# Optimization experiments

Hardware: AMD Instinct MI355X
Metric: run time of the kernel (lower is better)

The kernel has to match this reference:

```python
import jax, jax.numpy as jnp
import numpy as np

T, B, F = 160, 640, 40
HID, PROJ, LAYERS = 768, 256, 3


def lstm_proj_layer(x, Wk, b, Wp, reverse=False):
    # x: [T, B, in]; Wk: [in+PROJ, 4*HID]; b: [4*HID]; Wp: [HID, PROJ]
    nb = x.shape[1]
    c0 = jnp.zeros((nb, HID), x.dtype)
    h0 = jnp.zeros((nb, PROJ), x.dtype)

    def step(carry, xt):
        c, h = carry
        z = jnp.concatenate([xt, h], axis=-1) @ Wk + b
        i, j, f, o = jnp.split(z, 4, axis=-1)  # TF LSTMCell gate order i,j,f,o
        c = jax.nn.sigmoid(f + 1.0) * c + jax.nn.sigmoid(i) * jnp.tanh(j)  # forget_bias=1.0
        h = (jax.nn.sigmoid(o) * jnp.tanh(c)) @ Wp  # projection
        return (c, h), h

    _, ys = jax.lax.scan(step, (c0, h0), x, reverse=reverse)
    return ys  # [T, B, PROJ], time-aligned with input even when reverse=True


def _run_stack(x, params, reverse):
    for (Wk, b, Wp) in params:
        x = lstm_proj_layer(x, Wk, b, Wp, reverse=reverse)
    return x


def setup_inputs() -> dict:
    key = jax.random.key(0)
    keys = jax.random.split(key, 1 + 6 * LAYERS)
    inp = {"batch": jax.random.normal(keys[0], (T, B, F), dtype=jnp.float32)}
    ki = 1
    for d in ("fw", "bw"):
        for l in range(LAYERS):
            in_dim = F if l == 0 else PROJ
            inp[f"Wk_{d}{l}"] = jax.random.normal(keys[ki], (in_dim + PROJ, 4 * HID), dtype=jnp.float32) * 0.05
            inp[f"b_{d}{l}"] = jnp.zeros((4 * HID,), dtype=jnp.float32)
            inp[f"Wp_{d}{l}"] = jax.random.normal(keys[ki + 1], (HID, PROJ), dtype=jnp.float32) * 0.05
            ki += 2
    return inp


def reference(batch,
              Wk_fw0, b_fw0, Wp_fw0, Wk_fw1, b_fw1, Wp_fw1, Wk_fw2, b_fw2, Wp_fw2,
              Wk_bw0, b_bw0, Wp_bw0, Wk_bw1, b_bw1, Wp_bw1, Wk_bw2, b_bw2, Wp_bw2):
    fw_params = [(Wk_fw0, b_fw0, Wp_fw0), (Wk_fw1, b_fw1, Wp_fw1), (Wk_fw2, b_fw2, Wp_fw2)]
    bw_params = [(Wk_bw0, b_bw0, Wp_bw0), (Wk_bw1, b_bw1, Wp_bw1), (Wk_bw2, b_bw2, Wp_bw2)]
    out_fw = _run_stack(batch, fw_params, reverse=False)
    out_bw = _run_stack(batch, bw_params, reverse=True)
    outputs = jnp.concatenate([out_fw, out_bw], axis=2)  # [T, B, 2*PROJ]
    embedded = (outputs[0] + outputs[-1]) / 2.0
    # tf.nn.l2_normalize semantics
    embedded = embedded * jax.lax.rsqrt(jnp.maximum(jnp.sum(embedded * embedded, axis=-1, keepdims=True), 1e-12))
    return embedded
```

## Files before the change

### kernel.cpp

```cpp
#include <hip/hip_runtime.h>


typedef _Float16 h8 __attribute__((ext_vector_type(8)));
typedef float f4 __attribute__((ext_vector_type(4)));

#define T_STEPS 160
#define NB 640
#define HID 768
#define PROJ 256
#define NGATE 3072

__device__ __forceinline__ float sigm(float x) { return 1.0f / (1.0f + __expf(-x)); }
__device__ __forceinline__ float tanh_fast(float x) { return 2.0f / (1.0f + __expf(-2.0f * x)) - 1.0f; }

struct GateArgs {
  const _Float16* A0[6];
  const _Float16* A1[6];
  const _Float16* Bw[6];
  const float*    bias[6];
  float*          cst[6];
  _Float16*       g[6];
  int w0[6];
  int lda0[6];
  int K[6];
  int act[6];
};

struct ProjArgs {
  const _Float16* G[6];
  const _Float16* Wp[6];
  _Float16* out[6];
  _Float16* out2[6];
  int act[6];
};

__global__ __launch_bounds__(256, 3) void gate_step(GateArgs args) {
  const int z = blockIdx.z;
  if (!args.act[z]) return;

  __shared__ __align__(16) char sm[36864];
  _Float16 (*As)[72] = (_Float16(*)[72])sm;
  _Float16 (*Bs)[72] = (_Float16(*)[72])(sm + 18432);
  float (*zs)[65] = (float(*)[65])sm;

  const _Float16* A0 = args.A0[z];
  const _Float16* A1 = args.A1[z];
  const _Float16* Bw = args.Bw[z];
  const int w0 = args.w0[z], lda0 = args.lda0[z], K = args.K[z];
  const int n0 = blockIdx.x * 128;
  const int m0 = blockIdx.y * 128;
  const int tid = threadIdx.x;
  const int lane = tid & 63;
  const int wv = tid >> 6;
  const int wm = (wv & 1) * 64;
  const int wn = (wv >> 1) * 64;

  const float* bias = args.bias[z];
  float* cstate = args.cst[z];
  const int uu = tid & 15;
  const int rbase = tid >> 4;
  float cpre[2][8];
  float bpre[2][4];
#pragma unroll
  for (int p = 0; p < 2; ++p) {
    const int u0 = (n0 + p * 64) >> 2;
#pragma unroll
    for (int gg = 0; gg < 4; ++gg)
      bpre[p][gg] = bias[gg * HID + u0 + uu];
#pragma unroll
    for (int it = 0; it < 8; ++it)
      cpre[p][it] = cstate[(size_t)(m0 + it * 16 + rbase) * HID + u0 + uu];
  }

  f4 acc[4][4] = {};

  const int lr = tid >> 3;
  const int lkg = (tid & 7) * 8;

  h8 av[4], bv[4];
  {
    const int gk = lkg;
    if (gk < w0) {
#pragma unroll
      for (int r = 0; r < 4; ++r)
        av[r] = *(const h8*)(A0 + (size_t)(m0 + lr + 32 * r) * lda0 + gk);
    } else {
#pragma unroll
      for (int r = 0; r < 4; ++r)
        av[r] = *(const h8*)(A1 + (size_t)(m0 + lr + 32 * r) * 256 + (gk - w0));
    }
#pragma unroll
    for (int r = 0; r < 4; ++r)
      bv[r] = *(const h8*)(Bw + (size_t)(n0 + lr + 32 * r) * K + gk);
  }

  for (int k0 = 0; k0 < K; k0 += 64) {
    __syncthreads();
#pragma unroll
    for (int r = 0; r < 4; ++r) {
      *(h8*)&As[lr + 32 * r][lkg] = av[r];
      *(h8*)&Bs[lr + 32 * r][lkg] = bv[r];
    }
    if (k0 + 64 < K) {
      const int gk = k0 + 64 + lkg;
      if (gk < w0) {
#pragma unroll
        for (int r = 0; r < 4; ++r)
          av[r] = *(const h8*)(A0 + (size_t)(m0 + lr + 32 * r) * lda0 + gk);
      } else {
#pragma unroll
        for (int r = 0; r < 4; ++r)
          av[r] = *(const h8*)(A1 + (size_t)(m0 + lr + 32 * r) * 256 + (gk - w0));
      }
#pragma unroll
      for (int r = 0; r < 4; ++r)
        bv[r] = *(const h8*)(Bw + (size_t)(n0 + lr + 32 * r) * K + gk);
    }
    __syncthreads();
#pragma unroll
    for (int kk = 0; kk < 2; ++kk) {
      const int kq = ((lane >> 4) * 8) + kk * 32;
      h8 bf[4];
#pragma unroll
      for (int j = 0; j < 4; ++j)
        bf[j] = *(const h8*)&Bs[wn + (lane & 15) + 16 * j][kq];
#pragma unroll
      for (int i = 0; i < 4; ++i) {
        h8 af = *(const h8*)&As[wm + (lane & 15) + 16 * i][kq];
#pragma unroll
        for (int j = 0; j < 4; ++j)
          acc[i][j] = __builtin_amdgcn_mfma_f32_16x16x32_f16(af, bf[j], acc[i][j], 0, 0, 0);
      }
    }
  }

  _Float16* gout = args.g[z];
#pragma unroll
  for (int p = 0; p < 2; ++p) {
    __syncthreads();
    if ((wv >> 1) == p) {
#pragma unroll
      for (int mi = 0; mi < 4; ++mi)
#pragma unroll
        for (int ni = 0; ni < 4; ++ni)
#pragma unroll
          for (int r = 0; r < 4; ++r) {
            int row = wm + mi * 16 + ((lane >> 4) << 2) + r;
            int col = ni * 16 + (lane & 15);
            zs[row][col] = acc[mi][ni][r];
          }
    }
    __syncthreads();
    const int u0 = (n0 + p * 64) >> 2;
#pragma unroll
    for (int it = 0; it < 8; ++it) {
      int row = it * 16 + rbase;
      float zi = zs[row][4 * uu + 0] + bpre[p][0];
      float zj = zs[row][4 * uu + 1] + bpre[p][1];
      float zf = zs[row][4 * uu + 2] + bpre[p][2];
      float zo = zs[row][4 * uu + 3] + bpre[p][3];
      size_t co = (size_t)(m0 + row) * HID + u0 + uu;
      float cold = cpre[p][it];
      float cnew = sigm(zf + 1.0f) * cold + sigm(zi) * tanh_fast(zj);
      float g = sigm(zo) * tanh_fast(cnew);
      cstate[co] = cnew;
      gout[co] = (_Float16)g;
    }
  }
}

__global__ __launch_bounds__(256) void proj_step(ProjArgs args) {
  const int z = blockIdx.z;
  if (!args.act[z]) return;

  __shared__ __align__(16) _Float16 As[64][72];
  __shared__ __align__(16) _Float16 Bs[64][72];

  const _Float16* A = args.G[z];
  const _Float16* B = args.Wp[z];
  const int n0 = blockIdx.x * 64;
  const int m0 = blockIdx.y * 64;
  const int tid = threadIdx.x;
  const int lane = tid & 63;
  const int wv = tid >> 6;
  const int wm = (wv & 1) * 32;
  const int wn = (wv >> 1) * 32;

  f4 acc[2][2] = {};
  const int lr = tid >> 3;
  const int lkg = (tid & 7) * 8;

  h8 av0 = *(const h8*)(A + (size_t)(m0 + lr) * HID + lkg);
  h8 av1 = *(const h8*)(A + (size_t)(m0 + lr + 32) * HID + lkg);
  h8 bv0 = *(const h8*)(B + (size_t)(n0 + lr) * HID + lkg);
  h8 bv1 = *(const h8*)(B + (size_t)(n0 + lr + 32) * HID + lkg);

  for (int k0 = 0; k0 < HID; k0 += 64) {
    __syncthreads();
    *(h8*)&As[lr][lkg] = av0;
    *(h8*)&As[lr + 32][lkg] = av1;
    *(h8*)&Bs[lr][lkg] = bv0;
    *(h8*)&Bs[lr + 32][lkg] = bv1;
    if (k0 + 64 < HID) {
      const int gk = k0 + 64 + lkg;
      av0 = *(const h8*)(A + (size_t)(m0 + lr) * HID + gk);
      av1 = *(const h8*)(A + (size_t)(m0 + lr + 32) * HID + gk);
      bv0 = *(const h8*)(B + (size_t)(n0 + lr) * HID + gk);
      bv1 = *(const h8*)(B + (size_t)(n0 + lr + 32) * HID + gk);
    }
    __syncthreads();
    const int mr = wm + (lane & 15);
    const int nr = wn + (lane & 15);
#pragma unroll
    for (int kk = 0; kk < 2; ++kk) {
      const int kq = ((lane >> 4) * 8) + kk * 32;
      h8 a0 = *(const h8*)&As[mr][kq];
      h8 a1 = *(const h8*)&As[mr + 16][kq];
      h8 b0 = *(const h8*)&Bs[nr][kq];
      h8 b1 = *(const h8*)&Bs[nr + 16][kq];
      acc[0][0] = __builtin_amdgcn_mfma_f32_16x16x32_f16(a0, b0, acc[0][0], 0, 0, 0);
      acc[0][1] = __builtin_amdgcn_mfma_f32_16x16x32_f16(a0, b1, acc[0][1], 0, 0, 0);
      acc[1][0] = __builtin_amdgcn_mfma_f32_16x16x32_f16(a1, b0, acc[1][0], 0, 0, 0);
      acc[1][1] = __builtin_amdgcn_mfma_f32_16x16x32_f16(a1, b1, acc[1][1], 0, 0, 0);
    }
  }

  _Float16* outp = args.out[z];
  _Float16* out2 = args.out2[z];
#pragma unroll
  for (int mi = 0; mi < 2; ++mi)
#pragma unroll
    for (int ni = 0; ni < 2; ++ni)
#pragma unroll
      for (int r = 0; r < 4; ++r) {
        int row = wm + mi * 16 + ((lane >> 4) << 2) + r;
        int col = wn + ni * 16 + (lane & 15);
        _Float16 v = (_Float16)acc[mi][ni][r];
        size_t o = (size_t)(m0 + row) * PROJ + (n0 + col);
        outp[o] = v;
        if (out2) out2[o] = v;
      }
}

__global__ void convX(const float* __restrict__ X, _Float16* __restrict__ X16, size_t total) {
  size_t i = (size_t)blockIdx.x * 256 + threadIdx.x;
  if (i >= total) return;
  int p = (int)(i & 63);
  size_t tb = i >> 6;
  float v = (p < 40) ? X[tb * 40 + p] : 0.0f;
  X16[i] = (_Float16)v;
}

__global__ void conv_wk(const float* __restrict__ Wk, _Float16* __restrict__ out,
                        int mode, int Kpad, size_t total) {
  size_t i = (size_t)blockIdx.x * 256 + threadIdx.x;
  if (i >= total) return;
  int k = (int)(i % Kpad);
  int n = (int)(i / Kpad);
  int u = n >> 2, g = n & 3;
  int col = g * HID + u;
  float v;
  if (mode == 0) {
    if (k < 40)      v = Wk[(size_t)k * NGATE + col];
    else if (k < 64) v = 0.0f;
    else             v = Wk[(size_t)(k - 24) * NGATE + col];
  } else {
    v = Wk[(size_t)k * NGATE + col];
  }
  out[i] = (_Float16)v;
}

__global__ void conv_wp(const float* __restrict__ Wp, _Float16* __restrict__ out, size_t total) {
  size_t i = (size_t)blockIdx.x * 256 + threadIdx.x;
  if (i >= total) return;
  int k = (int)(i % HID);
  int c = (int)(i / HID);
  out[i] = (_Float16)Wp[(size_t)k * PROJ + c];
}

__global__ __launch_bounds__(256) void readout(const _Float16* __restrict__ E, float* __restrict__ out) {
  const size_t SL = (size_t)NB * PROJ;
  int b = blockIdx.x, tid = threadIdx.x;
  float v[2];
  float ss = 0.0f;
#pragma unroll
  for (int i = 0; i < 2; ++i) {
    int j = tid + i * 256;
    int d = j >> 8, c = j & 255;
    const _Float16* base = E + (size_t)d * 2 * SL;
    float a = (float)base[(size_t)b * PROJ + c];
    float zv = (float)base[SL + (size_t)b * PROJ + c];
    v[i] = 0.5f * (a + zv);
    ss += v[i] * v[i];
  }
#pragma unroll
  for (int off = 32; off; off >>= 1) ss += __shfl_down(ss, off);
  __shared__ float ps[4];
  if ((tid & 63) == 0) ps[tid >> 6] = ss;
  __syncthreads();
  float tot = ps[0] + ps[1] + ps[2] + ps[3];
  float nrm = rsqrtf(fmaxf(tot, 1e-12f));
  out[(size_t)b * 512 + tid] = v[0] * nrm;
  out[(size_t)b * 512 + tid + 256] = v[1] * nrm;
}

extern "C" void kernel_launch(void* const* d_in, const int* in_sizes, int n_in,
                              void* d_out, int out_size, void* d_ws, size_t ws_size,
                              hipStream_t stream) {
  (void)in_sizes; (void)n_in; (void)out_size; (void)ws_size;
  const float* X = (const float*)d_in[0];
  const float* Wk[2][3]; const float* Bi[2][3]; const float* Wp[2][3];
  for (int d = 0; d < 2; ++d)
    for (int l = 0; l < 3; ++l) {
      int base = 1 + d * 9 + l * 3;
      Wk[d][l] = (const float*)d_in[base];
      Bi[d][l] = (const float*)d_in[base + 1];
      Wp[d][l] = (const float*)d_in[base + 2];
    }

  char* ws = (char*)d_ws;
  size_t off = 0;
  auto alloc = [&](size_t bytes) -> void* {
    void* p = ws + off;
    off += (bytes + 255) & ~(size_t)255;
    return p;
  };

  const size_t SL = (size_t)NB * PROJ;

  _Float16* X16 = (_Float16*)alloc((size_t)T_STEPS * NB * 64 * 2);
  _Float16* WkT[2][3];
  for (int d = 0; d < 2; ++d)
    for (int l = 0; l < 3; ++l)
      WkT[d][l] = (_Float16*)alloc((size_t)NGATE * (l == 0 ? 320 : 512) * 2);
  _Float16* WpT[2][3];
  for (int d = 0; d < 2; ++d)
    for (int l = 0; l < 3; ++l)
      WpT[d][l] = (_Float16*)alloc((size_t)PROJ * HID * 2);
  _Float16* Hbuf = (_Float16*)alloc(6UL * 4 * SL * 2);
  float* cst = (float*)alloc(6UL * NB * HID * 4);
  _Float16* gbuf = (_Float16*)alloc(6UL * NB * HID * 2);
  _Float16* embed = (_Float16*)alloc(4UL * SL * 2);

  auto Hslot = [&](int l, int d, int slot) -> _Float16* {
    return Hbuf + (((size_t)(l * 2 + d) * 4) + slot) * SL;
  };

  {
    size_t tot = (size_t)T_STEPS * NB * 64;
    convX<<<dim3((unsigned)((tot + 255) / 256)), 256, 0, stream>>>(X, X16, tot);
  }
  for (int d = 0; d < 2; ++d)
    for (int l = 0; l < 3; ++l) {
      int Kpad = (l == 0) ? 320 : 512;
      size_t tot = (size_t)NGATE * Kpad;
      conv_wk<<<dim3((unsigned)((tot + 255) / 256)), 256, 0, stream>>>(
          Wk[d][l], WkT[d][l], (l == 0) ? 0 : 1, Kpad, tot);
      size_t totp = (size_t)PROJ * HID;
      conv_wp<<<dim3((unsigned)((totp + 255) / 256)), 256, 0, stream>>>(Wp[d][l], WpT[d][l], totp);
    }
  hipMemsetAsync(Hbuf, 0, 6UL * 4 * SL * 2, stream);
  hipMemsetAsync(cst, 0, 6UL * NB * HID * 4, stream);

  for (int s = 0; s <= 161; ++s) {
    GateArgs ga{};
    ProjArgs pa{};
    for (int l = 0; l < 3; ++l)
      for (int d = 0; d < 2; ++d) {
        int z = l * 2 + d;
        int t = s - l;
        if (t < 0 || t > 159) { ga.act[z] = 0; pa.act[z] = 0; continue; }
        int tt = (d == 0) ? t : 159 - t;
        ga.act[z] = 1; pa.act[z] = 1;
        if (l == 0) {
          ga.A0[z] = X16 + (size_t)tt * NB * 64;
          ga.w0[z] = 64; ga.lda0[z] = 64; ga.K[z] = 320;
        } else {
          ga.A0[z] = Hslot(l - 1, d, (tt + 1) & 3);
          ga.w0[z] = 256; ga.lda0[z] = 256; ga.K[z] = 512;
        }
        int rdslot = (d == 0) ? (tt & 3) : ((tt + 2) & 3);
        ga.A1[z] = Hslot(l, d, rdslot);
        ga.Bw[z] = WkT[d][l];
        ga.bias[z] = Bi[d][l];
        ga.cst[z] = cst + (size_t)z * NB * HID;
        ga.g[z] = gbuf + (size_t)z * NB * HID;

        pa.G[z] = gbuf + (size_t)z * NB * HID;
        pa.Wp[z] = WpT[d][l];
        pa.out[z] = Hslot(l, d, (tt + 1) & 3);
        pa.out2[z] = nullptr;
        if (l == 2 && (tt == 0 || tt == 159))
          pa.out2[z] = embed + ((size_t)d * 2 + (tt == 0 ? 0 : 1)) * SL;
      }
    gate_step<<<dim3(24, 5, 6), 256, 0, stream>>>(ga);
    proj_step<<<dim3(4, 10, 6), 256, 0, stream>>>(pa);
  }

  readout<<<dim3(NB), 256, 0, stream>>>(embed, (float*)d_out);
}
```

Baseline: 5.509 ms.

## Fuse gate and projection steps into one launch with flag-based dependencies

Merges the per-step gate and projection kernels into a single fused launch. Projection for step s-1 runs in a subset of the blocks and signals completion via atomic counters, while gate blocks for step s spin-wait on those counters before starting. The gate output buffer is double-buffered by parity so the two steps can overlap. This halves the launch count and lets projection and gate work overlap, at the cost of spin-wait latency and a dependence on every producer block being co-resident or already scheduled to avoid deadlock.

Result: slower. 7.312 ms (+32.7%).

```diff
diff --git a/kernel.cpp b/kernel.cpp
--- a/kernel.cpp
+++ b/kernel.cpp
@@ -9,36 +9,30 @@
 #define HID 768
 #define PROJ 256
 #define NGATE 3072
+#define SL ((size_t)NB * PROJ)
 
 __device__ __forceinline__ float sigm(float x) { return 1.0f / (1.0f + __expf(-x)); }
 __device__ __forceinline__ float tanh_fast(float x) { return 2.0f / (1.0f + __expf(-2.0f * x)) - 1.0f; }
 
-struct GateArgs {
+struct SArgs {
   const _Float16* A0[6];
   const _Float16* A1[6];
   const _Float16* Bw[6];
   const float*    bias[6];
   float*          cst[6];
-  _Float16*       g[6];
-  int w0[6];
-  int lda0[6];
-  int K[6];
-  int act[6];
-};
-
-struct ProjArgs {
+  _Float16*       gout[6];
+  int w0[6], lda0[6], K[6], gact[6];
+  int thrOwn[6], thrPrev[6];
   const _Float16* G[6];
   const _Float16* Wp[6];
-  _Float16* out[6];
+  _Float16* hout[6];
   _Float16* out2[6];
-  int act[6];
+  int pact[6];
+  int* flags;
 };
 
-__global__ __launch_bounds__(256, 3) void gate_step(GateArgs args) {
-  const int z = blockIdx.z;
-  if (!args.act[z]) return;
-
-  __shared__ __align__(16) char sm[36864];
+__device__ __forceinline__ void gate_body(char* sm, const SArgs& args, int z,
+                                          int bx, int by, int tid) {
   _Float16 (*As)[72] = (_Float16(*)[72])sm;
   _Float16 (*Bs)[72] = (_Float16(*)[72])(sm + 18432);
   float (*zs)[65] = (float(*)[65])sm;
@@ -47,9 +41,8 @@
   const _Float16* A1 = args.A1[z];
   const _Float16* Bw = args.Bw[z];
   const int w0 = args.w0[z], lda0 = args.lda0[z], K = args.K[z];
-  const int n0 = blockIdx.x * 128;
-  const int m0 = blockIdx.y * 128;
-  const int tid = threadIdx.x;
+  const int n0 = bx * 128;
+  const int m0 = by * 128;
   const int lane = tid & 63;
   const int wv = tid >> 6;
   const int wm = (wv & 1) * 64;
@@ -134,7 +127,7 @@
     }
   }
 
-  _Float16* gout = args.g[z];
+  _Float16* gout = args.gout[z];
 #pragma unroll
   for (int p = 0; p < 2; ++p) {
     __syncthreads();
@@ -169,18 +162,15 @@
   }
 }
 
-__global__ __launch_bounds__(256) void proj_step(ProjArgs args) {
-  const int z = blockIdx.z;
-  if (!args.act[z]) return;
-
-  __shared__ __align__(16) _Float16 As[64][72];
-  __shared__ __align__(16) _Float16 Bs[64][72];
+__device__ __forceinline__ void proj_body(char* sm, const SArgs& args, int z,
+                                          int bx, int by, int tid) {
+  _Float16 (*As)[72] = (_Float16(*)[72])sm;
+  _Float16 (*Bs)[72] = (_Float16(*)[72])(sm + 9216);
 
   const _Float16* A = args.G[z];
   const _Float16* B = args.Wp[z];
-  const int n0 = blockIdx.x * 64;
-  const int m0 = blockIdx.y * 64;
-  const int tid = threadIdx.x;
+  const int n0 = bx * 64;
+  const int m0 = by * 64;
   const int lane = tid & 63;
   const int wv = tid >> 6;
   const int wm = (wv & 1) * 32;
@@ -225,7 +215,7 @@
     }
   }
 
-  _Float16* outp = args.out[z];
+  _Float16* outp = args.hout[z];
   _Float16* out2 = args.out2[z];
 #pragma unroll
   for (int mi = 0; mi < 2; ++mi)
@@ -240,6 +230,46 @@
         outp[o] = v;
         if (out2) out2[o] = v;
       }
+}
+
+__global__ __launch_bounds__(256, 3) void step_fused(SArgs a) {
+  __shared__ __align__(16) char sm[36864];
+  const int b = blockIdx.x;
+  const int tid = threadIdx.x;
+
+  if (b % 3 == 0) {
+    const int pidx = b / 3;
+    const int pz = pidx / 40, prem = pidx % 40;
+    if (a.pact[pz]) {
+      proj_body(sm, a, pz, prem % 4, prem / 4, tid);
+      __syncthreads();
+      if (tid == 0)
+        __hip_atomic_fetch_add(&a.flags[pz * 32], 1,
+                               __ATOMIC_RELEASE, __HIP_MEMORY_SCOPE_SYSTEM);
+    }
+  }
+
+  const int gz = b / 120, grem = b % 120;
+  if (!a.gact[gz]) return;
+
+  if (tid == 0) {
+    const int th1 = a.thrOwn[gz], th2 = a.thrPrev[gz];
+    if (th1 > 0) {
+      int* f = &a.flags[gz * 32];
+      while (__hip_atomic_load(f, __ATOMIC_RELAXED, __HIP_MEMORY_SCOPE_SYSTEM) < th1)
+        __builtin_amdgcn_s_sleep(2);
+    }
+    if (th2 > 0) {
+      int* f = &a.flags[(gz - 2) * 32];
+      while (__hip_atomic_load(f, __ATOMIC_RELAXED, __HIP_MEMORY_SCOPE_SYSTEM) < th2)
+        __builtin_amdgcn_s_sleep(2);
+    }
+    if ((th1 | th2) != 0)
+      (void)__hip_atomic_load(&a.flags[gz * 32], __ATOMIC_ACQUIRE, __HIP_MEMORY_SCOPE_AGENT);
+  }
+  __syncthreads();
+
+  gate_body(sm, a, gz, grem % 24, grem / 24, tid);
 }
 
 __global__ void convX(const float* __restrict__ X, _Float16* __restrict__ X16, size_t total) {
@@ -279,7 +309,6 @@
 }
 
 __global__ __launch_bounds__(256) void readout(const _Float16* __restrict__ E, float* __restrict__ out) {
-  const size_t SL = (size_t)NB * PROJ;
   int b = blockIdx.x, tid = threadIdx.x;
   float v[2];
   float ss = 0.0f;
@@ -326,8 +355,6 @@
     return p;
   };
 
-  const size_t SL = (size_t)NB * PROJ;
-
   _Float16* X16 = (_Float16*)alloc((size_t)T_STEPS * NB * 64 * 2);
   _Float16* WkT[2][3];
   for (int d = 0; d < 2; ++d)
@@ -339,11 +366,15 @@
       WpT[d][l] = (_Float16*)alloc((size_t)PROJ * HID * 2);
   _Float16* Hbuf = (_Float16*)alloc(6UL * 4 * SL * 2);
   float* cst = (float*)alloc(6UL * NB * HID * 4);
-  _Float16* gbuf = (_Float16*)alloc(6UL * NB * HID * 2);
+  _Float16* gbuf = (_Float16*)alloc(2UL * 6 * NB * HID * 2);
   _Float16* embed = (_Float16*)alloc(4UL * SL * 2);
+  int* flags = (int*)alloc(6UL * 32 * 4);
 
   auto Hslot = [&](int l, int d, int slot) -> _Float16* {
     return Hbuf + (((size_t)(l * 2 + d) * 4) + slot) * SL;
+  };
+  auto Gbuf = [&](int parity, int z) -> _Float16* {
+    return gbuf + ((size_t)parity * 6 + z) * NB * HID;
   };
 
   {
@@ -361,40 +392,55 @@
     }
   hipMemsetAsync(Hbuf, 0, 6UL * 4 * SL * 2, stream);
   hipMemsetAsync(cst, 0, 6UL * NB * HID * 4, stream);
-
-  for (int s = 0; s <= 161; ++s) {
-    GateArgs ga{};
-    ProjArgs pa{};
+  hipMemsetAsync(flags, 0, 6UL * 32 * 4, stream);
+
+  int projdone[6] = {0, 0, 0, 0, 0, 0};
+  for (int s = 0; s <= 162; ++s) {
+    SArgs fa{};
+    fa.flags = flags;
+    const int u = s - 1;
     for (int l = 0; l < 3; ++l)
       for (int d = 0; d < 2; ++d) {
         int z = l * 2 + d;
-        int t = s - l;
-        if (t < 0 || t > 159) { ga.act[z] = 0; pa.act[z] = 0; continue; }
+        if (u < 0) { fa.pact[z] = 0; continue; }
+        int t = u - l;
+        if (t < 0 || t > 159) { fa.pact[z] = 0; continue; }
         int tt = (d == 0) ? t : 159 - t;
-        ga.act[z] = 1; pa.act[z] = 1;
-        if (l == 0) {
-          ga.A0[z] = X16 + (size_t)tt * NB * 64;
-          ga.w0[z] = 64; ga.lda0[z] = 64; ga.K[z] = 320;
-        } else {
-          ga.A0[z] = Hslot(l - 1, d, (tt + 1) & 3);
-          ga.w0[z] = 256; ga.lda0[z] = 256; ga.K[z] = 512;
+        fa.pact[z] = 1;
+        fa.G[z] = Gbuf(u & 1, z);
+        fa.Wp[z] = WpT[d][l];
+        fa.hout[z] = Hslot(l, d, (tt + 1) & 3);
+        fa.out2[z] = nullptr;
+        if (l == 2 && (tt == 0 || tt == 159))
+          fa.out2[z] = embed + ((size_t)d * 2 + (tt == 0 ? 0 : 1)) * SL;
+        projdone[z] += 40;
+      }
+    if (s <= 161) {
+      for (int l = 0; l < 3; ++l)
+        for (int d = 0; d < 2; ++d) {
+          int z = l * 2 + d;
+          int t = s - l;
+          if (t < 0 || t > 159) { fa.gact[z] = 0; continue; }
+          int tt = (d == 0) ? t : 159 - t;
+          fa.gact[z] = 1;
+          if (l == 0) {
+            fa.A0[z] = X16 + (size_t)tt * NB * 64;
+            fa.w0[z] = 64; fa.lda0[z] = 64; fa.K[z] = 320;
+          } else {
+            fa.A0[z] = Hslot(l - 1, d, (tt + 1) & 3);
+            fa.w0[z] = 256; fa.lda0[z] = 256; fa.K[z] = 512;
+          }
+          int rdslot = (d == 0) ? (tt & 3) : ((tt + 2) & 3);
+          fa.A1[z] = Hslot(l, d, rdslot);
+          fa.Bw[z] = WkT[d][l];
+          fa.bias[z] = Bi[d][l];
+          fa.cst[z] = cst + (size_t)z * NB * HID;
+          fa.gout[z] = Gbuf(s & 1, z);
+          fa.thrOwn[z] = projdone[z];
+          fa.thrPrev[z] = (l >= 1) ? projdone[z - 2] : 0;
         }
-        int rdslot = (d == 0) ? (tt & 3) : ((tt + 2) & 3);
-        ga.A1[z] = Hslot(l, d, rdslot);
-        ga.Bw[z] = WkT[d][l];
-        ga.bias[z] = Bi[d][l];
-        ga.cst[z] = cst + (size_t)z * NB * HID;
-        ga.g[z] = gbuf + (size_t)z * NB * HID;
-
-        pa.G[z] = gbuf + (size_t)z * NB * HID;
-        pa.Wp[z] = WpT[d][l];
-        pa.out[z] = Hslot(l, d, (tt + 1) & 3);
-        pa.out2[z] = nullptr;
-        if (l == 2 && (tt == 0 || tt == 159))
-          pa.out2[z] = embed + ((size_t)d * 2 + (tt == 0 ? 0 : 1)) * SL;
-      }
-    gate_step<<<dim3(24, 5, 6), 256, 0, stream>>>(ga);
-    proj_step<<<dim3(4, 10, 6), 256, 0, stream>>>(pa);
+    }
+    step_fused<<<dim3(720), 256, 0, stream>>>(fa);
   }
 
   readout<<<dim3(NB), 256, 0, stream>>>(embed, (float*)d_out);
```

## Interleave forward gate and backward projection in fused half-step kernels

Applied to the files above, without the earlier changes.

Replaces the separate per-step gate and projection launches with a single half_step kernel. Each launch runs the gate GEMMs of one direction alongside the projection GEMMs of the other direction, staggered by half a step. The aim is to fill the GPU with independent work and avoid a launch where only the small projection runs. This adds a branch on the block index and a shared-memory size sized for the larger gate tile, and relies on the offset schedule keeping the recurrences correct.

Result: slower. 6.245 ms (+13.4%).

```diff
diff --git a/kernel.cpp b/kernel.cpp
--- a/kernel.cpp
+++ b/kernel.cpp
@@ -9,54 +9,39 @@
 #define HID 768
 #define PROJ 256
 #define NGATE 3072
+#define SL ((size_t)NB * PROJ)
 
 __device__ __forceinline__ float sigm(float x) { return 1.0f / (1.0f + __expf(-x)); }
 __device__ __forceinline__ float tanh_fast(float x) { return 2.0f / (1.0f + __expf(-2.0f * x)) - 1.0f; }
 
-struct GateArgs {
-  const _Float16* A0[6];
-  const _Float16* A1[6];
-  const _Float16* Bw[6];
-  const float*    bias[6];
-  float*          cst[6];
-  _Float16*       g[6];
-  int w0[6];
-  int lda0[6];
-  int K[6];
-  int act[6];
+struct HArgs {
+  const _Float16* A0[3];
+  const _Float16* A1[3];
+  const _Float16* Bw[3];
+  const float*    bias[3];
+  float*          cst[3];
+  _Float16*       gout[3];
+  int w0[3], lda0[3], K[3], gact[3];
+  const _Float16* G[3];
+  const _Float16* Wp[3];
+  _Float16* hout[3];
+  _Float16* out2[3];
+  int pact[3];
 };
 
-struct ProjArgs {
-  const _Float16* G[6];
-  const _Float16* Wp[6];
-  _Float16* out[6];
-  _Float16* out2[6];
-  int act[6];
-};
-
-__global__ __launch_bounds__(256, 3) void gate_step(GateArgs args) {
-  const int z = blockIdx.z;
-  if (!args.act[z]) return;
-
-  __shared__ __align__(16) char sm[36864];
+__device__ __forceinline__ void gate_body(char* sm, const _Float16* A0, const _Float16* A1,
+                                          const _Float16* Bw, const float* bias,
+                                          float* cstate, _Float16* gout,
+                                          int w0, int lda0, int K, int n0, int m0, int tid) {
   _Float16 (*As)[72] = (_Float16(*)[72])sm;
   _Float16 (*Bs)[72] = (_Float16(*)[72])(sm + 18432);
   float (*zs)[65] = (float(*)[65])sm;
 
-  const _Float16* A0 = args.A0[z];
-  const _Float16* A1 = args.A1[z];
-  const _Float16* Bw = args.Bw[z];
-  const int w0 = args.w0[z], lda0 = args.lda0[z], K = args.K[z];
-  const int n0 = blockIdx.x * 128;
-  const int m0 = blockIdx.y * 128;
-  const int tid = threadIdx.x;
   const int lane = tid & 63;
   const int wv = tid >> 6;
   const int wm = (wv & 1) * 64;
   const int wn = (wv >> 1) * 64;
 
-  const float* bias = args.bias[z];
-  float* cstate = args.cst[z];
   const int uu = tid & 15;
   const int rbase = tid >> 4;
   float cpre[2][8];
@@ -134,7 +119,6 @@
     }
   }
 
-  _Float16* gout = args.g[z];
 #pragma unroll
   for (int p = 0; p < 2; ++p) {
     __syncthreads();
@@ -169,18 +153,12 @@
   }
 }
 
-__global__ __launch_bounds__(256) void proj_step(ProjArgs args) {
-  const int z = blockIdx.z;
-  if (!args.act[z]) return;
-
-  __shared__ __align__(16) _Float16 As[64][72];
-  __shared__ __align__(16) _Float16 Bs[64][72];
-
-  const _Float16* A = args.G[z];
-  const _Float16* B = args.Wp[z];
-  const int n0 = blockIdx.x * 64;
-  const int m0 = blockIdx.y * 64;
-  const int tid = threadIdx.x;
+__device__ __forceinline__ void proj_body(char* sm, const _Float16* A, const _Float16* B,
+                                          _Float16* outp, _Float16* out2,
+                                          int n0, int m0, int tid) {
+  _Float16 (*As)[72] = (_Float16(*)[72])sm;
+  _Float16 (*Bs)[72] = (_Float16(*)[72])(sm + 9216);
+
   const int lane = tid & 63;
   const int wv = tid >> 6;
   const int wm = (wv & 1) * 32;
@@ -225,8 +203,6 @@
     }
   }
 
-  _Float16* outp = args.out[z];
-  _Float16* out2 = args.out2[z];
 #pragma unroll
   for (int mi = 0; mi < 2; ++mi)
 #pragma unroll
@@ -240,6 +216,23 @@
         outp[o] = v;
         if (out2) out2[o] = v;
       }
+}
+
+__global__ __launch_bounds__(256, 3) void half_step(HArgs a) {
+  __shared__ __align__(16) char sm[36864];
+  const int tid = threadIdx.x;
+  const int bz = blockIdx.z;
+  if (bz < 3) {
+    if (!a.gact[bz]) return;
+    gate_body(sm, a.A0[bz], a.A1[bz], a.Bw[bz], a.bias[bz], a.cst[bz], a.gout[bz],
+              a.w0[bz], a.lda0[bz], a.K[bz], blockIdx.x * 128, blockIdx.y * 128, tid);
+  } else {
+    const int idx = blockIdx.x * 5 + blockIdx.y;
+    const int pi = idx / 40, tile = idx % 40;
+    if (!a.pact[pi]) return;
+    proj_body(sm, a.G[pi], a.Wp[pi], a.hout[pi], a.out2[pi],
+              (tile % 4) * 64, (tile / 4) * 64, tid);
+  }
 }
 
 __global__ void convX(const float* __restrict__ X, _Float16* __restrict__ X16, size_t total) {
@@ -279,7 +272,6 @@
 }
 
 __global__ __launch_bounds__(256) void readout(const _Float16* __restrict__ E, float* __restrict__ out) {
-  const size_t SL = (size_t)NB * PROJ;
   int b = blockIdx.x, tid = threadIdx.x;
   float v[2];
   float ss = 0.0f;
@@ -325,8 +317,6 @@
     off += (bytes + 255) & ~(size_t)255;
     return p;
   };
-
-  const size_t SL = (size_t)NB * PROJ;
 
   _Float16* X16 = (_Float16*)alloc((size_t)T_STEPS * NB * 64 * 2);
   _Float16* WkT[2][3];
@@ -362,39 +352,56 @@
   hipMemsetAsync(Hbuf, 0, 6UL * 4 * SL * 2, stream);
   hipMemsetAsync(cst, 0, 6UL * NB * HID * 4, stream);
 
-  for (int s = 0; s <= 161; ++s) {
-    GateArgs ga{};
-    ProjArgs pa{};
-    for (int l = 0; l < 3; ++l)
-      for (int d = 0; d < 2; ++d) {
-        int z = l * 2 + d;
-        int t = s - l;
-        if (t < 0 || t > 159) { ga.act[z] = 0; pa.act[z] = 0; continue; }
-        int tt = (d == 0) ? t : 159 - t;
-        ga.act[z] = 1; pa.act[z] = 1;
-        if (l == 0) {
-          ga.A0[z] = X16 + (size_t)tt * NB * 64;
-          ga.w0[z] = 64; ga.lda0[z] = 64; ga.K[z] = 320;
-        } else {
-          ga.A0[z] = Hslot(l - 1, d, (tt + 1) & 3);
-          ga.w0[z] = 256; ga.lda0[z] = 256; ga.K[z] = 512;
-        }
-        int rdslot = (d == 0) ? (tt & 3) : ((tt + 2) & 3);
-        ga.A1[z] = Hslot(l, d, rdslot);
-        ga.Bw[z] = WkT[d][l];
-        ga.bias[z] = Bi[d][l];
-        ga.cst[z] = cst + (size_t)z * NB * HID;
-        ga.g[z] = gbuf + (size_t)z * NB * HID;
-
-        pa.G[z] = gbuf + (size_t)z * NB * HID;
-        pa.Wp[z] = WpT[d][l];
-        pa.out[z] = Hslot(l, d, (tt + 1) & 3);
-        pa.out2[z] = nullptr;
-        if (l == 2 && (tt == 0 || tt == 159))
-          pa.out2[z] = embed + ((size_t)d * 2 + (tt == 0 ? 0 : 1)) * SL;
-      }
-    gate_step<<<dim3(24, 5, 6), 256, 0, stream>>>(ga);
-    proj_step<<<dim3(4, 10, 6), 256, 0, stream>>>(pa);
+  auto fill_gate = [&](HArgs& fa, int i, int l, int d, int s) {
+    int z = l * 2 + d;
+    int t = s - l;
+    if (t < 0 || t > 159) { fa.gact[i] = 0; return; }
+    int tt = (d == 0) ? t : 159 - t;
+    fa.gact[i] = 1;
+    if (l == 0) {
+      fa.A0[i] = X16 + (size_t)tt * NB * 64;
+      fa.w0[i] = 64; fa.lda0[i] = 64; fa.K[i] = 320;
+    } else {
+      fa.A0[i] = Hslot(l - 1, d, (tt + 1) & 3);
+      fa.w0[i] = 256; fa.lda0[i] = 256; fa.K[i] = 512;
+    }
+    int rdslot = (d == 0) ? (tt & 3) : ((tt + 2) & 3);
+    fa.A1[i] = Hslot(l, d, rdslot);
+    fa.Bw[i] = WkT[d][l];
+    fa.bias[i] = Bi[d][l];
+    fa.cst[i] = cst + (size_t)z * NB * HID;
+    fa.gout[i] = gbuf + (size_t)z * NB * HID;
+  };
+  auto fill_proj = [&](HArgs& fa, int i, int l, int d, int u) {
+    int z = l * 2 + d;
+    if (u < 0) { fa.pact[i] = 0; return; }
+    int t = u - l;
+    if (t < 0 || t > 159) { fa.pact[i] = 0; return; }
+    int tt = (d == 0) ? t : 159 - t;
+    fa.pact[i] = 1;
+    fa.G[i] = gbuf + (size_t)z * NB * HID;
+    fa.Wp[i] = WpT[d][l];
+    fa.hout[i] = Hslot(l, d, (tt + 1) & 3);
+    fa.out2[i] = nullptr;
+    if (l == 2 && (tt == 0 || tt == 159))
+      fa.out2[i] = embed + ((size_t)d * 2 + (tt == 0 ? 0 : 1)) * SL;
+  };
+
+  for (int s = 0; s <= 162; ++s) {
+    {
+      HArgs fa{};
+      bool any = false;
+      for (int l = 0; l < 3; ++l) { fill_gate(fa, l, l, 0, s); any |= (bool)fa.gact[l]; }
+      for (int l = 0; l < 3; ++l) { fill_proj(fa, l, l, 1, s - 1); any |= (bool)fa.pact[l]; }
+      if (any) half_step<<<dim3(24, 5, 4), 256, 0, stream>>>(fa);
+    }
+    {
+      HArgs fa{};
+      bool any = false;
+      for (int l = 0; l < 3; ++l) { fill_gate(fa, l, l, 1, s); any |= (bool)fa.gact[l]; }
+      for (int l = 0; l < 3; ++l) { fill_proj(fa, l, l, 0, s); any |= (bool)fa.pact[l]; }
+      if (any) half_step<<<dim3(24, 5, 4), 256, 0, stream>>>(fa);
+    }
   }
 
   readout<<<dim3(NB), 256, 0, stream>>>(embed, (float*)d_out);
```
